# Performance work log

Measured on AMD Instinct MI355X. Metric: run time of the kernel, lower is better.

Reference implementation:

```python
import jax, jax.numpy as jnp
import numpy as np

L = 4            # n_layers
D_MODEL = 768
D_STATE = 16
D_CONV = 4
EXPAND = 2
D_INNER = EXPAND * D_MODEL      # 1536
DT_RANK = (D_MODEL + 15) // 16  # 48
B = 2
T = 2048
LN_EPS = 1e-5


def setup_inputs() -> dict:
    key = jax.random.key(0)
    ks = jax.random.split(key, 12)
    s = 0.02
    x = jax.random.normal(ks[0], (B, T, D_MODEL), dtype=jnp.float32)
    in_proj_w = jax.random.normal(ks[1], (L, 2 * D_INNER, D_MODEL), dtype=jnp.float32) * s
    conv_w = jax.random.normal(ks[2], (L, D_INNER, D_CONV), dtype=jnp.float32) * s
    conv_b = jnp.zeros((L, D_INNER), dtype=jnp.float32)
    x_proj_w = jax.random.normal(ks[3], (L, DT_RANK + 2 * D_STATE, D_INNER), dtype=jnp.float32) * s
    dt_proj_w = jax.random.normal(ks[4], (L, D_INNER, DT_RANK), dtype=jnp.float32) * s
    dt_proj_b = jax.random.normal(ks[5], (L, D_INNER), dtype=jnp.float32) * 0.1
    # Standard S4D-real init: A = -[1..d_state], stored as log
    A_log = jnp.log(jnp.broadcast_to(
        jnp.arange(1, D_STATE + 1, dtype=jnp.float32), (L, D_INNER, D_STATE)))
    D_param = jnp.ones((L, D_INNER), dtype=jnp.float32)
    out_proj_w = jax.random.normal(ks[6], (L, D_MODEL, D_INNER), dtype=jnp.float32) * s
    ln_g = jnp.ones((L, D_MODEL), dtype=jnp.float32)
    ln_b = jnp.zeros((L, D_MODEL), dtype=jnp.float32)
    return {"x": x, "in_proj_w": in_proj_w, "conv_w": conv_w, "conv_b": conv_b,
            "x_proj_w": x_proj_w, "dt_proj_w": dt_proj_w, "dt_proj_b": dt_proj_b,
            "A_log": A_log, "D_param": D_param, "out_proj_w": out_proj_w,
            "ln_g": ln_g, "ln_b": ln_b}


def _layernorm(x, g, b):
    mu = jnp.mean(x, axis=-1, keepdims=True)
    var = jnp.mean(jnp.square(x - mu), axis=-1, keepdims=True)
    return (x - mu) * jax.lax.rsqrt(var + LN_EPS) * g + b


def _mamba_layer(x, inw, convw, convb, xpw, dtw, dtb, A_log, Dp, outw):
    # x: [B,T,d_model]
    Tn = x.shape[1]
    xz = jnp.einsum('btd,ed->bte', x, inw)          # [B,T,2*d_inner]
    xin, z = jnp.split(xz, 2, axis=-1)              # each [B,T,d_inner]
    # causal depthwise conv1d over time (kernel d_conv)
    xp = jnp.pad(xin, ((0, 0), (D_CONV - 1, 0), (0, 0)))
    xc = convb
    for k in range(D_CONV):
        xc = xc + xp[:, k:k + Tn, :] * convw[:, k]
    xc = jax.nn.silu(xc)                            # [B,T,d_inner]
    dbl = jnp.einsum('bti,ei->bte', xc, xpw)        # [B,T,dt_rank+2*d_state]
    dt, Bs, Cs = jnp.split(dbl, [DT_RANK, DT_RANK + D_STATE], axis=-1)
    dt = jax.nn.softplus(jnp.einsum('btr,dr->btd', dt, dtw) + dtb)  # [B,T,d_inner]
    A = -jnp.exp(A_log)                             # [d_inner,d_state]
    dA = jnp.exp(jnp.einsum('btd,dn->btdn', dt, A))  # discretized A
    dBu = (dt * xc)[..., None] * Bs[:, :, None, :]   # [B,T,d_inner,d_state]

    def step(h, inp):
        dA_t, dBu_t, C_t = inp                      # [B,d,n],[B,d,n],[B,n]
        h = dA_t * h + dBu_t
        y = jnp.einsum('bdn,bn->bd', h, C_t)
        return h, y

    h0 = jnp.zeros((x.shape[0], D_INNER, D_STATE), x.dtype)
    _, ys = jax.lax.scan(step, h0,
                         (jnp.swapaxes(dA, 0, 1), jnp.swapaxes(dBu, 0, 1),
                          jnp.swapaxes(Cs, 0, 1)))
    y = jnp.swapaxes(ys, 0, 1) + xc * Dp            # skip connection D*u
    y = y * jax.nn.silu(z)                          # gate
    return jnp.einsum('bti,ei->bte', y, outw)       # [B,T,d_model]


def reference(x, in_proj_w, conv_w, conv_b, x_proj_w, dt_proj_w, dt_proj_b,
              A_log, D_param, out_proj_w, ln_g, ln_b):
    for l in range(L):
        residual = x
        h = _mamba_layer(x, in_proj_w[l], conv_w[l], conv_b[l], x_proj_w[l],
                         dt_proj_w[l], dt_proj_b[l], A_log[l], D_param[l],
                         out_proj_w[l])
        h = _layernorm(h, ln_g[l], ln_b[l])
        x = h + residual                            # dropout=0 -> identity
    return x
```

## Files before the change

### kernel.cpp

```cpp
#include <hip/hip_runtime.h>

#define T_LEN 2048
#define DM    768
#define DI    1536
#define DS    16
#define BB    2
#define NROWS (BB * T_LEN)
#define NCH   128
#define CLEN  16
#define NSEG  8
#define SEGC  16

#define OFF_DTB 0
#define OFF_A   6144
#define OFF_DP  104448
#define OFF_CW  110592
#define OFF_CB  135168
#define OFF_LG  141312
#define OFF_LB  144384
#define PRM_TOT 147456

typedef __attribute__((ext_vector_type(8))) short bh8;
typedef __attribute__((ext_vector_type(4))) float f32x4;

typedef const __attribute__((address_space(1))) void as1_void;
typedef __attribute__((address_space(3))) void as3_void;

__device__ __forceinline__ void glds16(const void* g, void* l) {
    __builtin_amdgcn_global_load_lds((as1_void*)g, (as3_void*)l, 16, 0, 0);
}

__device__ __forceinline__ float bf2f(unsigned short u) {
    return __uint_as_float(((unsigned)u) << 16);
}
__device__ __forceinline__ unsigned short f2bf(float f) {
    unsigned u = __float_as_uint(f);
    u += 0x7FFFu + ((u >> 16) & 1u);
    return (unsigned short)(u >> 16);
}

__device__ __forceinline__ void ld8(const void* p, long e0, int bf, float* v) {
    if (bf) {
        bh8 u = *(const bh8*)((const unsigned short*)p + e0);
#pragma unroll
        for (int j = 0; j < 8; ++j) v[j] = bf2f((unsigned short)u[j]);
    } else {
        const f32x4* q = (const f32x4*)((const float*)p + e0);
        f32x4 a = q[0], b = q[1];
#pragma unroll
        for (int j = 0; j < 4; ++j) { v[j] = a[j]; v[4 + j] = b[j]; }
    }
}

__device__ __forceinline__ void cp8(unsigned short* dst, long de0,
                                    const void* src, long se0, int bf) {
    if (bf) {
        *(bh8*)&dst[de0] = *(const bh8*)((const unsigned short*)src + se0);
    } else {
        const f32x4* q = (const f32x4*)((const float*)src + se0);
        f32x4 a = q[0], b = q[1];
        bh8 o;
#pragma unroll
        for (int j = 0; j < 4; ++j) { o[j] = (short)f2bf(a[j]); o[4 + j] = (short)f2bf(b[j]); }
        *(bh8*)&dst[de0] = o;
    }
}

__global__ void k_sniff(const unsigned short* __restrict__ x, int* __restrict__ flag) {
    __shared__ int cnt[4];
    int tid = threadIdx.x;
    int local = 0;
#pragma unroll
    for (int j = 0; j < 4; ++j) {
        unsigned short u = x[tid * 4 + j];
        int e = (u >> 7) & 0xFF;
        if (e >= 100 && e <= 140) local++;
    }
    for (int off = 32; off; off >>= 1) local += __shfl_down(local, off, 64);
    if ((tid & 63) == 0) cnt[tid >> 6] = local;
    __syncthreads();
    if (tid == 0) {
        int tot = cnt[0] + cnt[1] + cnt[2] + cnt[3];
        *flag = (tot >= 900) ? 1 : 0;
    }
}

__global__ void k_prep(const void* in_x, const void* in_inw, const void* in_ow,
                       const void* in_xpw, const void* in_dtw,
                       const void* dtb, const void* alog, const void* dpar,
                       const void* cw, const void* cb, const void* lg, const void* lb,
                       unsigned short* __restrict__ xbf, float* __restrict__ xf,
                       unsigned short* __restrict__ Win, unsigned short* __restrict__ Wout,
                       unsigned short* __restrict__ Wxp, unsigned short* __restrict__ Wdt,
                       float* __restrict__ prm, const int* __restrict__ flag) {
    const long G0 = 393216L;
    const long G1 = G0 + 1179648L;
    const long G2 = G1 + 589824L;
    const long G3 = G2 + 98304L;
    const long G4 = G3 + 49152L;
    const long G5 = G4 + 18432L;
    int bf = *flag;
    long g = (long)blockIdx.x * 256 + threadIdx.x;
    if (g >= G5) return;
    if (g < G0) {
        long e0 = g * 8;
        float v[8];
        ld8(in_x, e0, bf, v);
        bh8 o;
#pragma unroll
        for (int j = 0; j < 8; ++j) o[j] = (short)f2bf(v[j]);
        *(bh8*)&xbf[e0] = o;
        f32x4 a, b;
#pragma unroll
        for (int j = 0; j < 4; ++j) { a[j] = v[j]; b[j] = v[4 + j]; }
        ((f32x4*)&xf[e0])[0] = a;
        ((f32x4*)&xf[e0])[1] = b;
    } else if (g < G1) {
        long e0 = (g - G0) * 8;
        cp8(Win, e0, in_inw, e0, bf);
    } else if (g < G2) {
        long e0 = (g - G1) * 8;
        cp8(Wout, e0, in_ow, e0, bf);
    } else if (g < G3) {
        long e0 = (g - G2) * 8;
        int c = (int)(e0 % 1536);
        long rl = e0 / 1536;
        int r = (int)(rl % 128);
        int l = (int)(rl / 128);
        if (r < 80) cp8(Wxp, e0, in_xpw, ((long)l * 80 + r) * 1536 + c, bf);
        else        *(bh8*)&Wxp[e0] = (bh8)(short)0;
    } else if (g < G4) {
        long e0 = (g - G3) * 8;
        int c = (int)(e0 & 63);
        long rl = e0 >> 6;
        int d = (int)(rl % 1536);
        int l = (int)(rl / 1536);
        if (c < 48) cp8(Wdt, e0, in_dtw, ((long)l * 1536 + d) * 48 + c, bf);
        else        *(bh8*)&Wdt[e0] = (bh8)(short)0;
    } else {
        long e0 = (g - G4) * 8;
        float v[8];
        if (e0 < OFF_A)        ld8(dtb,  e0 - OFF_DTB, bf, v);
        else if (e0 < OFF_DP) {
            ld8(alog, e0 - OFF_A, bf, v);
#pragma unroll
            for (int j = 0; j < 8; ++j) v[j] = -__expf(v[j]);
        }
        else if (e0 < OFF_CW)  ld8(dpar, e0 - OFF_DP, bf, v);
        else if (e0 < OFF_CB)  ld8(cw,   e0 - OFF_CW, bf, v);
        else if (e0 < OFF_LG)  ld8(cb,   e0 - OFF_CB, bf, v);
        else if (e0 < OFF_LB)  ld8(lg,   e0 - OFF_LG, bf, v);
        else                   ld8(lb,   e0 - OFF_LB, bf, v);
        f32x4 a, b;
#pragma unroll
        for (int j = 0; j < 4; ++j) { a[j] = v[j]; b[j] = v[4 + j]; }
        ((f32x4*)&prm[e0])[0] = a;
        ((f32x4*)&prm[e0])[1] = b;
    }
}

__global__ __launch_bounds__(256) void k_gemm128(const unsigned short* __restrict__ A,
                                                 const unsigned short* __restrict__ B,
                                                 unsigned short* __restrict__ C,
                                                 int M, int N, int K) {
    __shared__ __align__(16) unsigned short As[128 * 32];
    __shared__ __align__(16) unsigned short Bs[128 * 32];
    const int tid = threadIdx.x;
    const int lane = tid & 63, wid = tid >> 6;
    const int wm = wid >> 1, wn = wid & 1;
    const long arow0 = (long)blockIdx.y * 128;
    const long bcol0 = (long)blockIdx.x * 128;
    const int r16 = lane >> 2;
    const int c8  = (lane & 3) * 8;
    f32x4 acc[4][4] = {};

    for (int k0 = 0; k0 < K; k0 += 32) {
#pragma unroll
        for (int j = 0; j < 2; ++j) {
            int chunk = wid + j * 4;
            int row = chunk * 16 + r16;
            glds16(&A[(arow0 + row) * K + k0 + c8], &As[chunk * 512]);
            glds16(&B[(bcol0 + row) * K + k0 + c8], &Bs[chunk * 512]);
        }
        __syncthreads();
        const int row = lane & 15, q8 = (lane >> 4) * 8;
        bh8 af[4], bfr[4];
#pragma unroll
        for (int i = 0; i < 4; ++i) af[i] = *(const bh8*)&As[(wm * 64 + i * 16 + row) * 32 + q8];
#pragma unroll
        for (int i = 0; i < 4; ++i) bfr[i] = *(const bh8*)&Bs[(wn * 64 + i * 16 + row) * 32 + q8];
#pragma unroll
        for (int i = 0; i < 4; ++i)
#pragma unroll
            for (int j = 0; j < 4; ++j)
                acc[i][j] = __builtin_amdgcn_mfma_f32_16x16x32_bf16(af[i], bfr[j], acc[i][j], 0, 0, 0);
        __syncthreads();
    }
    const int crow = (lane >> 4) * 4, ccol = lane & 15;
#pragma unroll
    for (int i = 0; i < 4; ++i)
#pragma unroll
        for (int j = 0; j < 4; ++j)
#pragma unroll
            for (int r = 0; r < 4; ++r) {
                long gr = arow0 + wm * 64 + i * 16 + crow + r;
                long gc = bcol0 + wn * 64 + j * 16 + ccol;
                C[gr * N + gc] = f2bf(acc[i][j][r]);
            }
}

__global__ __launch_bounds__(256) void k_xproj(const unsigned short* __restrict__ xz,
                                               const unsigned short* __restrict__ B,
                                               const float* __restrict__ cw,
                                               const float* __restrict__ cb,
                                               float* __restrict__ C) {
    __shared__ __align__(16) unsigned short As[64 * 32];
    __shared__ __align__(16) unsigned short Bs[64 * 32];
    const int tid = threadIdx.x;
    const int lane = tid & 63, w = tid >> 6;
    const int wm = w >> 1, wn = w & 1;
    const long arow0 = (long)blockIdx.y * 64;
    const long bcol0 = (long)blockIdx.x * 64;
    const int kbase = blockIdx.z * 384;
    const int r4 = lane >> 2;
    const int c8 = (lane & 3) * 8;
    const int t_o = tid >> 2;
    const int dl  = (tid & 3) * 8;
    const int sp  = (int)((arow0 + t_o) & (T_LEN - 1));
    f32x4 acc[2][2] = {};

    for (int kk = 0; kk < 384; kk += 32) {
        const int k0 = kbase + kk;
        glds16(&B[(bcol0 + w * 16 + r4) * DI + k0 + c8], &Bs[w * 512]);
        const int dg = k0 + dl;
        float xv[4][8];
#pragma unroll
        for (int rr = 0; rr < 4; ++rr) {
            if (sp - 3 + rr >= 0) {
                bh8 u = *(const bh8*)&xz[(arow0 + t_o - 3 + rr) * 3072 + dg];
#pragma unroll
                for (int q = 0; q < 8; ++q) xv[rr][q] = bf2f((unsigned short)u[q]);
            } else {
#pragma unroll
                for (int q = 0; q < 8; ++q) xv[rr][q] = 0.f;
            }
        }
        bh8 o;
#pragma unroll
        for (int q = 0; q < 8; ++q) {
            const f32x4 w4 = *(const f32x4*)&cw[(dg + q) * 4];
            float a = cb[dg + q] + w4[0] * xv[0][q] + w4[1] * xv[1][q]
                                 + w4[2] * xv[2][q] + w4[3] * xv[3][q];
            a = a / (1.f + __expf(-a));
            o[q] = (short)f2bf(a);
        }
        *(bh8*)&As[t_o * 32 + dl] = o;
        __syncthreads();
        const int row2 = lane & 15, q8 = (lane >> 4) * 8;
        bh8 af[2], bfr[2];
#pragma unroll
        for (int i = 0; i < 2; ++i) af[i] = *(const bh8*)&As[(wm * 32 + i * 16 + row2) * 32 + q8];
#pragma unroll
        for (int i = 0; i < 2; ++i) bfr[i] = *(const bh8*)&Bs[(wn * 32 + i * 16 + row2) * 32 + q8];
#pragma unroll
        for (int i = 0; i < 2; ++i)
#pragma unroll
            for (int j = 0; j < 2; ++j)
                acc[i][j] = __builtin_amdgcn_mfma_f32_16x16x32_bf16(af[i], bfr[j], acc[i][j], 0, 0, 0);
        __syncthreads();
    }
    const int crow = (lane >> 4) * 4, ccol = lane & 15;
#pragma unroll
    for (int i = 0; i < 2; ++i)
#pragma unroll
        for (int j = 0; j < 2; ++j)
#pragma unroll
            for (int r = 0; r < 4; ++r) {
                long gr = arow0 + wm * 32 + i * 16 + crow + r;
                long gc = bcol0 + wn * 32 + j * 16 + ccol;
                atomicAdd(&C[gr * 128 + gc], acc[i][j][r]);
            }
}

__global__ __launch_bounds__(256) void k_dtproj(const float* __restrict__ Dbl,
                                                const unsigned short* __restrict__ Wdt,
                                                const float* __restrict__ bias,
                                                unsigned short* __restrict__ Dt) {
    __shared__ __align__(16) unsigned short As[2 * 64 * 32];
    __shared__ __align__(16) unsigned short Bs[2 * 64 * 32];
    const int tid = threadIdx.x;
    const int lane = tid & 63, wid = tid >> 6;
    const int wm = wid >> 1, wn = wid & 1;
    const long arow0 = (long)blockIdx.y * 64;
    const long bcol0 = (long)blockIdx.x * 64;

    {
        int r = tid >> 2;
        int cs = (tid & 3) * 16;
        unsigned short tmp[16];
#pragma unroll
        for (int q = 0; q < 4; ++q) {
            int col0 = cs + q * 4;
            if (col0 < 48) {
                f32x4 v = *(const f32x4*)&Dbl[(arow0 + r) * 128 + col0];
#pragma unroll
                for (int j = 0; j < 4; ++j) tmp[q * 4 + j] = f2bf(v[j]);
            } else {
#pragma unroll
                for (int j = 0; j < 4; ++j) tmp[q * 4 + j] = 0;
            }
        }
        int p = cs >> 5;
        int cp = cs & 31;
        *(bh8*)&As[p * 2048 + r * 32 + cp]     = *(bh8*)&tmp[0];
        *(bh8*)&As[p * 2048 + r * 32 + cp + 8] = *(bh8*)&tmp[8];
    }
#pragma unroll
    for (int j = 0; j < 2; ++j) {
        int chunk = tid + j * 256;
        int p = chunk >> 8;
        int rem = chunk & 255;
        int row = rem >> 2;
        int c4 = rem & 3;
        glds16(&Wdt[(bcol0 + row) * 64 + p * 32 + c4 * 8], &Bs[chunk * 8]);
    }
    __syncthreads();

    const int row2 = lane & 15, q8 = (lane >> 4) * 8;
    f32x4 acc[2][2] = {};
#pragma unroll
    for (int p = 0; p < 2; ++p) {
        bh8 af[2], bfr[2];
#pragma unroll
        for (int i = 0; i < 2; ++i) af[i] = *(const bh8*)&As[p * 2048 + (wm * 32 + i * 16 + row2) * 32 + q8];
#pragma unroll
        for (int i = 0; i < 2; ++i) bfr[i] = *(const bh8*)&Bs[p * 2048 + (wn * 32 + i * 16 + row2) * 32 + q8];
#pragma unroll
        for (int i = 0; i < 2; ++i)
#pragma unroll
            for (int j = 0; j < 2; ++j)
                acc[i][j] = __builtin_amdgcn_mfma_f32_16x16x32_bf16(af[i], bfr[j], acc[i][j], 0, 0, 0);
    }
    const int crow = (lane >> 4) * 4, ccol = lane & 15;
#pragma unroll
    for (int i = 0; i < 2; ++i)
#pragma unroll
        for (int j = 0; j < 2; ++j)
#pragma unroll
            for (int r = 0; r < 4; ++r) {
                long gr = arow0 + wm * 32 + i * 16 + crow + r;
                long gc = bcol0 + wn * 32 + j * 16 + ccol;
                float v = acc[i][j][r] + bias[gc];
                v = (v > 20.f) ? v : log1pf(__expf(v));
                Dt[gr * DI + gc] = f2bf(v);
            }
}

__global__ __launch_bounds__(256) void k_outproj(const unsigned short* __restrict__ A,
                                                 const unsigned short* __restrict__ B,
                                                 float* __restrict__ C) {
    __shared__ __align__(16) unsigned short As[64 * 32];
    __shared__ __align__(16) unsigned short Bs[64 * 32];
    const int tid = threadIdx.x;
    const int lane = tid & 63, wid = tid >> 6;
    const int wm = wid >> 1, wn = wid & 1;
    const long arow0 = (long)blockIdx.y * 64;
    const long bcol0 = (long)blockIdx.x * 64;
    const int r16 = lane >> 2;
    const int c8  = (lane & 3) * 8;
    f32x4 acc[2][2] = {};

    for (int k0 = 0; k0 < DI; k0 += 32) {
        int row = wid * 16 + r16;
        glds16(&A[(arow0 + row) * DI + k0 + c8], &As[wid * 512]);
        glds16(&B[(bcol0 + row) * DI + k0 + c8], &Bs[wid * 512]);
        __syncthreads();
        const int row2 = lane & 15, q8 = (lane >> 4) * 8;
        bh8 af[2], bfr[2];
#pragma unroll
        for (int i = 0; i < 2; ++i) af[i] = *(const bh8*)&As[(wm * 32 + i * 16 + row2) * 32 + q8];
#pragma unroll
        for (int i = 0; i < 2; ++i) bfr[i] = *(const bh8*)&Bs[(wn * 32 + i * 16 + row2) * 32 + q8];
#pragma unroll
        for (int i = 0; i < 2; ++i)
#pragma unroll
            for (int j = 0; j < 2; ++j)
                acc[i][j] = __builtin_amdgcn_mfma_f32_16x16x32_bf16(af[i], bfr[j], acc[i][j], 0, 0, 0);
        __syncthreads();
    }
    const int crow = (lane >> 4) * 4, ccol = lane & 15;
#pragma unroll
    for (int i = 0; i < 2; ++i)
#pragma unroll
        for (int j = 0; j < 2; ++j)
#pragma unroll
            for (int r = 0; r < 4; ++r) {
                long gr = arow0 + wm * 32 + i * 16 + crow + r;
                long gc = bcol0 + wn * 32 + j * 16 + ccol;
                C[gr * DM + gc] = acc[i][j][r];
            }
}

__global__ __launch_bounds__(256) void k_scan1(const unsigned short* __restrict__ dt,
                                               const unsigned short* __restrict__ xz,
                                               const float* __restrict__ dbl,
                                               const float* __restrict__ An,
                                               const float* __restrict__ cw,
                                               const float* __restrict__ cb,
                                               float* __restrict__ hch,
                                               float* __restrict__ sdtb) {
    const int tid = threadIdx.x;
    const int db = blockIdx.x % 6;
    const int c  = (blockIdx.x / 6) % NCH;
    const int b  = blockIdx.x / (6 * NCH);
    const int d  = db * 256 + tid;
    const int t0 = c * CLEN;
    float h[DS], An_r[DS];
    const f32x4* Ap = (const f32x4*)(An + (long)d * DS);
#pragma unroll
    for (int q = 0; q < 4; ++q) {
        f32x4 a4 = Ap[q];
#pragma unroll
        for (int j = 0; j < 4; ++j) { An_r[q * 4 + j] = a4[j]; h[q * 4 + j] = 0.f; }
    }
    const f32x4 w4 = *(const f32x4*)&cw[d * 4];
    const float cbv = cb[d];
    const long rowb = (long)b * T_LEN + t0;
    float x1, x2, x3;
    if (c == 0) { x1 = x2 = x3 = 0.f; }
    else {
        x1 = bf2f(xz[(rowb - 1) * 3072 + d]);
        x2 = bf2f(xz[(rowb - 2) * 3072 + d]);
        x3 = bf2f(xz[(rowb - 3) * 3072 + d]);
    }
    float sdt = 0.f;
#pragma unroll 4
    for (int s = 0; s < CLEN; ++s) {
        long bt = rowb + s;
        float xt = bf2f(xz[bt * 3072 + d]);
        float a = cbv + w4[0] * x3 + w4[1] * x2 + w4[2] * x1 + w4[3] * xt;
        float xcv = a / (1.f + __expf(-a));
        x3 = x2; x2 = x1; x1 = xt;
        float dtv = bf2f(dt[bt * DI + d]);
        int bi = __builtin_amdgcn_readfirstlane((int)(bt * 128 + 48));
        const f32x4* bp = (const f32x4*)(dbl + bi);
        float Bv[DS];
#pragma unroll
        for (int q = 0; q < 4; ++q) {
            f32x4 b4 = bp[q];
#pragma unroll
            for (int j = 0; j < 4; ++j) Bv[q * 4 + j] = b4[j];
        }
        float du = dtv * xcv;
        sdt += dtv;
#pragma unroll
        for (int n = 0; n < DS; ++n)
            h[n] = __expf(An_r[n] * dtv) * h[n] + du * Bv[n];
    }
    long o = (((long)b * NCH + c) * DI + d) * DS;
    f32x4* hp = (f32x4*)(hch + o);
#pragma unroll
    for (int q = 0; q < 4; ++q) {
        f32x4 h4;
#pragma unroll
        for (int j = 0; j < 4; ++j) h4[j] = h[q * 4 + j];
        hp[q] = h4;
    }
    sdtb[((long)b * NCH + c) * DI + d] = sdt;
}

__global__ __launch_bounds__(256) void k_scan2a(float* __restrict__ hbuf,
                                                const float* __restrict__ sdtb,
                                                const float* __restrict__ An,
                                                float* __restrict__ cum,
                                                float* __restrict__ Gseg,
                                                float* __restrict__ Sseg) {
    long gid = (long)blockIdx.x * 256 + threadIdx.x;
    int n = (int)(gid & 15);
    long t = gid >> 4;
    int d  = (int)(t % DI);
    int sg = (int)((t / DI) & (NSEG - 1));
    int b  = (int)(t / (DI * NSEG));
    float an = An[(long)d * DS + n];
    float h = 0.f, cs = 0.f;
    for (int i = 0; i < SEGC; ++i) {
        int c = sg * SEGC + i;
        long rowi = ((long)b * NCH + c) * DI + d;
        long idx = rowi * DS + n;
        float sdt = sdtb[rowi];
        float g = hbuf[idx];
        hbuf[idx] = h;
        if (n == 0) cum[rowi] = cs;
        h = __expf(an * sdt) * h + g;
        cs += sdt;
    }
    long gi = (((long)b * NSEG + sg) * DI + d) * DS + n;
    Gseg[gi] = h;
    if (n == 0) Sseg[((long)b * NSEG + sg) * DI + d] = cs;
}

__global__ __launch_bounds__(256) void k_scan3(const unsigned short* __restrict__ dt,
                                               const unsigned short* __restrict__ xz,
                                               const float* __restrict__ dbl,
                                               const float* __restrict__ An,
                                               const float* __restrict__ cw,
                                               const float* __restrict__ cb,
                                               const float* __restrict__ Dp,
                                               const float* __restrict__ hpref,
                                               const float* __restrict__ cum,
                                               const float* __restrict__ Gseg,
                                               const float* __restrict__ Sseg,
                                               unsigned short* __restrict__ ybf) {
    const int tid = threadIdx.x;
    const int db = blockIdx.x % 6;
    const int c  = (blockIdx.x / 6) % NCH;
    const int b  = blockIdx.x / (6 * NCH);
    const int d  = db * 256 + tid;
    const int t0 = c * CLEN;
    const int sg = c / SEGC;
    float h[DS], An_r[DS];
    long rowi = ((long)b * NCH + c) * DI + d;
    long o = rowi * DS;
    const float cs = cum[rowi];
    const f32x4* Ap = (const f32x4*)(An + (long)d * DS);
#pragma unroll
    for (int q = 0; q < 4; ++q) {
        f32x4 a4 = Ap[q];
#pragma unroll
        for (int j = 0; j < 4; ++j) An_r[q * 4 + j] = a4[j];
    }
    float Hn[DS];
#pragma unroll
    for (int n = 0; n < DS; ++n) Hn[n] = 0.f;
    for (int s2 = 0; s2 < sg; ++s2) {
        long gi = (((long)b * NSEG + s2) * DI + d) * DS;
        float S = Sseg[((long)b * NSEG + s2) * DI + d];
        const f32x4* Gp = (const f32x4*)(Gseg + gi);
#pragma unroll
        for (int q = 0; q < 4; ++q) {
            f32x4 g4 = Gp[q];
#pragma unroll
            for (int j = 0; j < 4; ++j) {
                int n = q * 4 + j;
                Hn[n] = __expf(An_r[n] * S) * Hn[n] + g4[j];
            }
        }
    }
    const f32x4* Pp = (const f32x4*)(hpref + o);
#pragma unroll
    for (int q = 0; q < 4; ++q) {
        f32x4 p4 = Pp[q];
#pragma unroll
        for (int j = 0; j < 4; ++j) {
            int n = q * 4 + j;
            h[n] = __expf(An_r[n] * cs) * Hn[n] + p4[j];
        }
    }
    const float dcoef = Dp[d];
    const f32x4 w4 = *(const f32x4*)&cw[d * 4];
    const float cbv = cb[d];
    const long rowb = (long)b * T_LEN + t0;
    float x1, x2, x3;
    if (c == 0) { x1 = x2 = x3 = 0.f; }
    else {
        x1 = bf2f(xz[(rowb - 1) * 3072 + d]);
        x2 = bf2f(xz[(rowb - 2) * 3072 + d]);
        x3 = bf2f(xz[(rowb - 3) * 3072 + d]);
    }
#pragma unroll 4
    for (int s = 0; s < CLEN; ++s) {
        long bt = rowb + s;
        float xt = bf2f(xz[bt * 3072 + d]);
        float a = cbv + w4[0] * x3 + w4[1] * x2 + w4[2] * x1 + w4[3] * xt;
        float xcv = a / (1.f + __expf(-a));
        x3 = x2; x2 = x1; x1 = xt;
        float dtv = bf2f(dt[bt * DI + d]);
        int bi = __builtin_amdgcn_readfirstlane((int)(bt * 128 + 48));
        const f32x4* bp = (const f32x4*)(dbl + bi);
        float Bv[DS], Cv[DS];
#pragma unroll
        for (int q = 0; q < 4; ++q) {
            f32x4 b4 = bp[q], c4 = bp[q + 4];
#pragma unroll
            for (int j = 0; j < 4; ++j) { Bv[q * 4 + j] = b4[j]; Cv[q * 4 + j] = c4[j]; }
        }
        float du = dtv * xcv;
        float yp[4] = {xcv * dcoef, 0.f, 0.f, 0.f};
#pragma unroll
        for (int n = 0; n < DS; ++n) {
            h[n] = __expf(An_r[n] * dtv) * h[n] + du * Bv[n];
            yp[n & 3] += h[n] * Cv[n];
        }
        float y = (yp[0] + yp[1]) + (yp[2] + yp[3]);
        float zv = bf2f(xz[bt * 3072 + DI + d]);
        y *= zv / (1.f + __expf(-zv));
        ybf[bt * DI + d] = f2bf(y);
    }
}

__global__ __launch_bounds__(256) void k_ln(const float* __restrict__ prj,
                                            float* __restrict__ x,
                                            unsigned short* __restrict__ xbf,
                                            const float* __restrict__ lg,
                                            const float* __restrict__ lb,
                                            void* __restrict__ dout,
                                            int is_last, const int* __restrict__ flag) {
    __shared__ float red[8];
    const int row = blockIdx.x;
    const int tid = threadIdx.x;
    float v[3];
    float s = 0.f, s2 = 0.f;
#pragma unroll
    for (int j = 0; j < 3; ++j) {
        v[j] = prj[(long)row * DM + tid + j * 256];
        s += v[j];
        s2 += v[j] * v[j];
    }
    for (int off = 32; off; off >>= 1) {
        s  += __shfl_down(s, off, 64);
        s2 += __shfl_down(s2, off, 64);
    }
    if ((tid & 63) == 0) { red[tid >> 6] = s; red[4 + (tid >> 6)] = s2; }
    __syncthreads();
    float S  = red[0] + red[1] + red[2] + red[3];
    float S2 = red[4] + red[5] + red[6] + red[7];
    float mu = S * (1.f / DM);
    float var = S2 * (1.f / DM) - mu * mu;
    float rs = rsqrtf(var + 1e-5f);
    int bf = *flag;
#pragma unroll
    for (int j = 0; j < 3; ++j) {
        int e = tid + j * 256;
        long idx = (long)row * DM + e;
        float out = (v[j] - mu) * rs * lg[e] + lb[e] + x[idx];
        x[idx] = out;
        xbf[idx] = f2bf(out);
        if (is_last) {
            if (bf) ((unsigned short*)dout)[idx] = f2bf(out);
            else    ((float*)dout)[idx] = out;
        }
    }
}

extern "C" void kernel_launch(void* const* d_in, const int* in_sizes, int n_in,
                              void* d_out, int out_size, void* d_ws, size_t ws_size,
                              hipStream_t stream) {
    char* ws = (char*)d_ws;
    const size_t O_FLAG = 0;
    const size_t O_WIN  = 256;
    const size_t O_WXP  = O_WIN  + 18874368;
    const size_t O_WDT  = O_WXP  + 1572864;
    const size_t O_WOUT = O_WDT  + 786432;
    const size_t O_PRM  = O_WOUT + 9437184;
    const size_t O_XBF  = O_PRM  + 589824;
    const size_t O_XF   = O_XBF  + 6291456;
    const size_t O_XZ   = O_XF   + 12582912;
    const size_t O_DBL  = O_XZ   + 25165824;
    const size_t O_DT   = O_DBL  + 2097152;
    const size_t O_HCH  = O_DT   + 12582912;
    const size_t O_SDT  = O_HCH  + 25165824;
    const size_t O_CUM  = O_SDT  + 1572864;
    const size_t O_GSEG = O_CUM  + 1572864;
    const size_t O_SSEG = O_GSEG + 1572864;
    const size_t O_YBF  = O_SSEG + 98304;

    int* flag = (int*)(ws + O_FLAG);
    unsigned short* Win  = (unsigned short*)(ws + O_WIN);
    unsigned short* Wxp  = (unsigned short*)(ws + O_WXP);
    unsigned short* Wdt  = (unsigned short*)(ws + O_WDT);
    unsigned short* Wout = (unsigned short*)(ws + O_WOUT);
    float* prm = (float*)(ws + O_PRM);
    unsigned short* Xbf = (unsigned short*)(ws + O_XBF);
    float* Xf  = (float*)(ws + O_XF);
    unsigned short* Xz = (unsigned short*)(ws + O_XZ);
    float* Dbl = (float*)(ws + O_DBL);
    unsigned short* Dt = (unsigned short*)(ws + O_DT);
    float* Hch = (float*)(ws + O_HCH);
    float* Sdt = (float*)(ws + O_SDT);
    float* Cum = (float*)(ws + O_CUM);
    float* Gsg = (float*)(ws + O_GSEG);
    float* Ssg = (float*)(ws + O_SSEG);
    unsigned short* Ybf = (unsigned short*)(ws + O_YBF);
    float* Prj = (float*)(ws + O_XZ);

    k_sniff<<<1, 256, 0, stream>>>((const unsigned short*)d_in[0], flag);
    k_prep<<<9096, 256, 0, stream>>>(d_in[0], d_in[1], d_in[9], d_in[4], d_in[5],
                                     d_in[6], d_in[7], d_in[8], d_in[2], d_in[3],
                                     d_in[10], d_in[11],
                                     Xbf, Xf, Win, Wout, Wxp, Wdt, prm, flag);

    for (int l = 0; l < 4; ++l) {
        const unsigned short* winL  = Win  + (size_t)l * 3072 * 768;
        const unsigned short* wxpL  = Wxp  + (size_t)l * 128 * 1536;
        const unsigned short* wdtL  = Wdt  + (size_t)l * 1536 * 64;
        const unsigned short* woutL = Wout + (size_t)l * 768 * 1536;
        const float* cwL  = prm + OFF_CW  + (size_t)l * DI * 4;
        const float* cbL  = prm + OFF_CB  + (size_t)l * DI;
        const float* dtbL = prm + OFF_DTB + (size_t)l * DI;
        const float* anL  = prm + OFF_A   + (size_t)l * DI * DS;
        const float* dpL  = prm + OFF_DP  + (size_t)l * DI;
        const float* lgL  = prm + OFF_LG  + (size_t)l * DM;
        const float* lbL  = prm + OFF_LB  + (size_t)l * DM;

        k_gemm128<<<dim3(24, 32), 256, 0, stream>>>(Xbf, winL, Xz, NROWS, 2 * DI, DM);
        hipMemsetAsync(Dbl, 0, 2097152, stream);
        k_xproj<<<dim3(2, 64, 4), 256, 0, stream>>>(Xz, wxpL, cwL, cbL, Dbl);
        k_dtproj<<<dim3(24, 64), 256, 0, stream>>>(Dbl, wdtL, dtbL, Dt);
        k_scan1<<<BB * NCH * 6, 256, 0, stream>>>(Dt, Xz, Dbl, anL, cwL, cbL, Hch, Sdt);
        k_scan2a<<<1536, 256, 0, stream>>>(Hch, Sdt, anL, Cum, Gsg, Ssg);
        k_scan3<<<BB * NCH * 6, 256, 0, stream>>>(Dt, Xz, Dbl, anL, cwL, cbL, dpL,
                                                  Hch, Cum, Gsg, Ssg, Ybf);
        k_outproj<<<dim3(12, 64), 256, 0, stream>>>(Ybf, woutL, Prj);
        k_ln<<<4096, 256, 0, stream>>>(Prj, Xf, Xbf, lgL, lbL, d_out, (l == 3) ? 1 : 0, flag);
    }
}
```

Measured before the change: 969.1 us.

## Retune scan chunking, stage B/C in LDS, swizzle GEMM blocks, fold memset

```diff
diff --git a/kernel.cpp b/kernel.cpp
--- a/kernel.cpp
+++ b/kernel.cpp
@@ -6,10 +6,10 @@
 #define DS    16
 #define BB    2
 #define NROWS (BB * T_LEN)
-#define NCH   128
-#define CLEN  16
+#define NCH   64
+#define CLEN  32
 #define NSEG  8
-#define SEGC  16
+#define SEGC  8
 
 #define OFF_DTB 0
 #define OFF_A   6144
@@ -92,16 +92,18 @@
                        unsigned short* __restrict__ xbf, float* __restrict__ xf,
                        unsigned short* __restrict__ Win, unsigned short* __restrict__ Wout,
                        unsigned short* __restrict__ Wxp, unsigned short* __restrict__ Wdt,
-                       float* __restrict__ prm, const int* __restrict__ flag) {
+                       float* __restrict__ prm, float* __restrict__ dblz,
+                       const int* __restrict__ flag) {
     const long G0 = 393216L;
     const long G1 = G0 + 1179648L;
     const long G2 = G1 + 589824L;
     const long G3 = G2 + 98304L;
     const long G4 = G3 + 49152L;
     const long G5 = G4 + 18432L;
+    const long G6 = G5 + 65536L;
     int bf = *flag;
     long g = (long)blockIdx.x * 256 + threadIdx.x;
-    if (g >= G5) return;
+    if (g >= G6) return;
     if (g < G0) {
         long e0 = g * 8;
         float v[8];
@@ -137,7 +139,7 @@
         int l = (int)(rl / 1536);
         if (c < 48) cp8(Wdt, e0, in_dtw, ((long)l * 1536 + d) * 48 + c, bf);
         else        *(bh8*)&Wdt[e0] = (bh8)(short)0;
-    } else {
+    } else if (g < G5) {
         long e0 = (g - G4) * 8;
         float v[8];
         if (e0 < OFF_A)        ld8(dtb,  e0 - OFF_DTB, bf, v);
@@ -156,6 +158,11 @@
         for (int j = 0; j < 4; ++j) { a[j] = v[j]; b[j] = v[4 + j]; }
         ((f32x4*)&prm[e0])[0] = a;
         ((f32x4*)&prm[e0])[1] = b;
+    } else {
+        long e0 = (g - G5) * 8;
+        f32x4 z = {0.f, 0.f, 0.f, 0.f};
+        ((f32x4*)&dblz[e0])[0] = z;
+        ((f32x4*)&dblz[e0])[1] = z;
     }
 }
 
@@ -168,8 +175,12 @@
     const int tid = threadIdx.x;
     const int lane = tid & 63, wid = tid >> 6;
     const int wm = wid >> 1, wn = wid & 1;
-    const long arow0 = (long)blockIdx.y * 128;
-    const long bcol0 = (long)blockIdx.x * 128;
+    const int id = blockIdx.y * 24 + blockIdx.x;
+    const int xcd = id & 7, loc = id >> 3;
+    const int bx = (xcd & 1) * 12 + loc % 12;
+    const int by = (xcd >> 1) * 8 + loc / 12;
+    const long arow0 = (long)by * 128;
+    const long bcol0 = (long)bx * 128;
     const int r16 = lane >> 2;
     const int c8  = (lane & 3) * 8;
     f32x4 acc[4][4] = {};
@@ -364,8 +375,12 @@
     const int tid = threadIdx.x;
     const int lane = tid & 63, wid = tid >> 6;
     const int wm = wid >> 1, wn = wid & 1;
-    const long arow0 = (long)blockIdx.y * 64;
-    const long bcol0 = (long)blockIdx.x * 64;
+    const int id = blockIdx.y * 12 + blockIdx.x;
+    const int xcd = id & 7, loc = id >> 3;
+    const int bx = (xcd & 1) * 6 + loc % 6;
+    const int by = (xcd >> 1) * 16 + loc / 6;
+    const long arow0 = (long)by * 64;
+    const long bcol0 = (long)bx * 64;
     const int r16 = lane >> 2;
     const int c8  = (lane & 3) * 8;
     f32x4 acc[2][2] = {};
@@ -409,12 +424,20 @@
                                                const float* __restrict__ cb,
                                                float* __restrict__ hch,
                                                float* __restrict__ sdtb) {
+    __shared__ __align__(16) float Bsh[CLEN * 16];
     const int tid = threadIdx.x;
+    const int lane = tid & 63, w = tid >> 6;
     const int db = blockIdx.x % 6;
     const int c  = (blockIdx.x / 6) % NCH;
     const int b  = blockIdx.x / (6 * NCH);
     const int d  = db * 256 + tid;
     const int t0 = c * CLEN;
+    const long rowb = (long)b * T_LEN + t0;
+    if (w < 2) {
+        int t = w * 16 + (lane >> 2);
+        int nq = lane & 3;
+        glds16(&dbl[(rowb + t) * 128 + 48 + nq * 4], &Bsh[w * 256]);
+    }
     float h[DS], An_r[DS];
     const f32x4* Ap = (const f32x4*)(An + (long)d * DS);
 #pragma unroll
@@ -425,7 +448,6 @@
     }
     const f32x4 w4 = *(const f32x4*)&cw[d * 4];
     const float cbv = cb[d];
-    const long rowb = (long)b * T_LEN + t0;
     float x1, x2, x3;
     if (c == 0) { x1 = x2 = x3 = 0.f; }
     else {
@@ -433,6 +455,7 @@
         x2 = bf2f(xz[(rowb - 2) * 3072 + d]);
         x3 = bf2f(xz[(rowb - 3) * 3072 + d]);
     }
+    __syncthreads();
     float sdt = 0.f;
 #pragma unroll 4
     for (int s = 0; s < CLEN; ++s) {
@@ -442,20 +465,18 @@
         float xcv = a / (1.f + __expf(-a));
         x3 = x2; x2 = x1; x1 = xt;
         float dtv = bf2f(dt[bt * DI + d]);
-        int bi = __builtin_amdgcn_readfirstlane((int)(bt * 128 + 48));
-        const f32x4* bp = (const f32x4*)(dbl + bi);
-        float Bv[DS];
+        const f32x4* bp = (const f32x4*)&Bsh[s * 16];
+        float du = dtv * xcv;
+        sdt += dtv;
 #pragma unroll
         for (int q = 0; q < 4; ++q) {
             f32x4 b4 = bp[q];
 #pragma unroll
-            for (int j = 0; j < 4; ++j) Bv[q * 4 + j] = b4[j];
-        }
-        float du = dtv * xcv;
-        sdt += dtv;
-#pragma unroll
-        for (int n = 0; n < DS; ++n)
-            h[n] = __expf(An_r[n] * dtv) * h[n] + du * Bv[n];
+            for (int j = 0; j < 4; ++j) {
+                int n = q * 4 + j;
+                h[n] = __expf(An_r[n] * dtv) * h[n] + du * b4[j];
+            }
+        }
     }
     long o = (((long)b * NCH + c) * DI + d) * DS;
     f32x4* hp = (f32x4*)(hch + o);
@@ -511,13 +532,24 @@
                                                const float* __restrict__ Gseg,
                                                const float* __restrict__ Sseg,
                                                unsigned short* __restrict__ ybf) {
+    __shared__ __align__(16) float Bsh[CLEN * 16];
+    __shared__ __align__(16) float Csh[CLEN * 16];
     const int tid = threadIdx.x;
+    const int lane = tid & 63, w = tid >> 6;
     const int db = blockIdx.x % 6;
     const int c  = (blockIdx.x / 6) % NCH;
     const int b  = blockIdx.x / (6 * NCH);
     const int d  = db * 256 + tid;
     const int t0 = c * CLEN;
     const int sg = c / SEGC;
+    const long rowb = (long)b * T_LEN + t0;
+    if (w < 2) {
+        int t = w * 16 + (lane >> 2);
+        glds16(&dbl[(rowb + t) * 128 + 48 + (lane & 3) * 4], &Bsh[w * 256]);
+    } else {
+        int t = (w - 2) * 16 + (lane >> 2);
+        glds16(&dbl[(rowb + t) * 128 + 64 + (lane & 3) * 4], &Csh[(w - 2) * 256]);
+    }
     float h[DS], An_r[DS];
     long rowi = ((long)b * NCH + c) * DI + d;
     long o = rowi * DS;
@@ -559,7 +591,6 @@
     const float dcoef = Dp[d];
     const f32x4 w4 = *(const f32x4*)&cw[d * 4];
     const float cbv = cb[d];
-    const long rowb = (long)b * T_LEN + t0;
     float x1, x2, x3;
     if (c == 0) { x1 = x2 = x3 = 0.f; }
     else {
@@ -567,6 +598,7 @@
         x2 = bf2f(xz[(rowb - 2) * 3072 + d]);
         x3 = bf2f(xz[(rowb - 3) * 3072 + d]);
     }
+    __syncthreads();
 #pragma unroll 4
     for (int s = 0; s < CLEN; ++s) {
         long bt = rowb + s;
@@ -575,21 +607,19 @@
         float xcv = a / (1.f + __expf(-a));
         x3 = x2; x2 = x1; x1 = xt;
         float dtv = bf2f(dt[bt * DI + d]);
-        int bi = __builtin_amdgcn_readfirstlane((int)(bt * 128 + 48));
-        const f32x4* bp = (const f32x4*)(dbl + bi);
-        float Bv[DS], Cv[DS];
-#pragma unroll
-        for (int q = 0; q < 4; ++q) {
-            f32x4 b4 = bp[q], c4 = bp[q + 4];
-#pragma unroll
-            for (int j = 0; j < 4; ++j) { Bv[q * 4 + j] = b4[j]; Cv[q * 4 + j] = c4[j]; }
-        }
+        const f32x4* bp = (const f32x4*)&Bsh[s * 16];
+        const f32x4* cp = (const f32x4*)&Csh[s * 16];
         float du = dtv * xcv;
         float yp[4] = {xcv * dcoef, 0.f, 0.f, 0.f};
 #pragma unroll
-        for (int n = 0; n < DS; ++n) {
-            h[n] = __expf(An_r[n] * dtv) * h[n] + du * Bv[n];
-            yp[n & 3] += h[n] * Cv[n];
+        for (int q = 0; q < 4; ++q) {
+            f32x4 b4 = bp[q], c4 = cp[q];
+#pragma unroll
+            for (int j = 0; j < 4; ++j) {
+                int n = q * 4 + j;
+                h[n] = __expf(An_r[n] * dtv) * h[n] + du * b4[j];
+                yp[j] += h[n] * c4[j];
+            }
         }
         float y = (yp[0] + yp[1]) + (yp[2] + yp[3]);
         float zv = bf2f(xz[bt * 3072 + DI + d]);
@@ -604,6 +634,7 @@
                                             const float* __restrict__ lg,
                                             const float* __restrict__ lb,
                                             void* __restrict__ dout,
+                                            float* __restrict__ dblz,
                                             int is_last, const int* __restrict__ flag) {
     __shared__ float red[8];
     const int row = blockIdx.x;
@@ -640,6 +671,8 @@
             else    ((float*)dout)[idx] = out;
         }
     }
+    long gid = (long)row * 256 + tid;
+    if (gid < 524288) dblz[gid] = 0.f;
 }
 
 extern "C" void kernel_launch(void* const* d_in, const int* in_sizes, int n_in,
@@ -658,9 +691,9 @@
     const size_t O_DBL  = O_XZ   + 25165824;
     const size_t O_DT   = O_DBL  + 2097152;
     const size_t O_HCH  = O_DT   + 12582912;
-    const size_t O_SDT  = O_HCH  + 25165824;
-    const size_t O_CUM  = O_SDT  + 1572864;
-    const size_t O_GSEG = O_CUM  + 1572864;
+    const size_t O_SDT  = O_HCH  + 12582912;
+    const size_t O_CUM  = O_SDT  + 786432;
+    const size_t O_GSEG = O_CUM  + 786432;
     const size_t O_SSEG = O_GSEG + 1572864;
     const size_t O_YBF  = O_SSEG + 98304;
 
@@ -684,10 +717,10 @@
     float* Prj = (float*)(ws + O_XZ);
 
     k_sniff<<<1, 256, 0, stream>>>((const unsigned short*)d_in[0], flag);
-    k_prep<<<9096, 256, 0, stream>>>(d_in[0], d_in[1], d_in[9], d_in[4], d_in[5],
+    k_prep<<<9352, 256, 0, stream>>>(d_in[0], d_in[1], d_in[9], d_in[4], d_in[5],
                                      d_in[6], d_in[7], d_in[8], d_in[2], d_in[3],
                                      d_in[10], d_in[11],
-                                     Xbf, Xf, Win, Wout, Wxp, Wdt, prm, flag);
+                                     Xbf, Xf, Win, Wout, Wxp, Wdt, prm, Dbl, flag);
 
     for (int l = 0; l < 4; ++l) {
         const unsigned short* winL  = Win  + (size_t)l * 3072 * 768;
@@ -703,7 +736,6 @@
         const float* lbL  = prm + OFF_LB  + (size_t)l * DM;
 
         k_gemm128<<<dim3(24, 32), 256, 0, stream>>>(Xbf, winL, Xz, NROWS, 2 * DI, DM);
-        hipMemsetAsync(Dbl, 0, 2097152, stream);
         k_xproj<<<dim3(2, 64, 4), 256, 0, stream>>>(Xz, wxpL, cwL, cbL, Dbl);
         k_dtproj<<<dim3(24, 64), 256, 0, stream>>>(Dbl, wdtL, dtbL, Dt);
         k_scan1<<<BB * NCH * 6, 256, 0, stream>>>(Dt, Xz, Dbl, anL, cwL, cbL, Hch, Sdt);
@@ -711,6 +743,7 @@
         k_scan3<<<BB * NCH * 6, 256, 0, stream>>>(Dt, Xz, Dbl, anL, cwL, cbL, dpL,
                                                   Hch, Cum, Gsg, Ssg, Ybf);
         k_outproj<<<dim3(12, 64), 256, 0, stream>>>(Ybf, woutL, Prj);
-        k_ln<<<4096, 256, 0, stream>>>(Prj, Xf, Xbf, lgL, lbL, d_out, (l == 3) ? 1 : 0, flag);
-    }
-}
+        k_ln<<<4096, 256, 0, stream>>>(Prj, Xf, Xbf, lgL, lbL, d_out, Dbl,
+                                       (l == 3) ? 1 : 0, flag);
+    }
+}
```

Result: faster. 935.1 us (-3.5%).
